# Kernel tuning notes

Hardware: AMD Instinct MI355X
Metric: run time of the kernel (lower is better)

Reference implementation:

```python
import jax, jax.numpy as jnp
import numpy as np

N = 500_000   # active voxel sites
C = 128       # inplanes == outplanes
K = 4         # 2x2 submanifold filter offsets
EPS = 1e-4    # SCN BatchNorm default eps


def setup_inputs() -> dict:
    key = jax.random.key(0)
    ks = jax.random.split(key, 10)
    feat = jax.random.normal(ks[0], (N, C), jnp.float32)
    in_idx = jax.random.randint(ks[1], (K, N), 0, N, dtype=jnp.int32)
    out_idx = jax.random.randint(ks[2], (K, N), 0, N, dtype=jnp.int32)
    mask = jax.random.randint(ks[3], (K, N), 0, 2, dtype=jnp.int32)
    scale = 1.0 / np.sqrt(K * C)
    W1 = jax.random.normal(ks[4], (K, C, C), jnp.float32) * scale
    W2 = jax.random.normal(ks[5], (K, C, C), jnp.float32) * scale
    gamma1 = jnp.ones((C,), jnp.float32)
    beta1 = jnp.zeros((C,), jnp.float32)
    mean1 = jax.random.normal(ks[6], (C,), jnp.float32) * 0.1
    var1 = jax.random.uniform(ks[7], (C,), jnp.float32, 0.5, 1.5)
    gamma2 = jnp.ones((C,), jnp.float32)
    beta2 = jnp.zeros((C,), jnp.float32)
    mean2 = jax.random.normal(ks[8], (C,), jnp.float32) * 0.1
    var2 = jax.random.uniform(ks[9], (C,), jnp.float32, 0.5, 1.5)
    return dict(feat=feat, W1=W1, W2=W2, gamma1=gamma1, beta1=beta1,
                mean1=mean1, var1=var1, gamma2=gamma2, beta2=beta2,
                mean2=mean2, var2=var2, in_idx=in_idx, out_idx=out_idx, mask=mask)


def _subm_conv(feat, W, in_idx, out_idx, maskf):
    # rulebook gather -> GEMM -> scatter-add, one pass per kernel offset
    out = jnp.zeros((feat.shape[0], W.shape[-1]), feat.dtype)
    for k in range(W.shape[0]):  # K=4 fixed small offsets
        g = feat[in_idx[k]] * maskf[k][:, None]   # [N, Cin]
        out = out.at[out_idx[k]].add(g @ W[k])    # scatter to active sites
    return out


def _bn(x, gamma, beta, mean, var):
    return (x - mean) * jax.lax.rsqrt(var + EPS) * gamma + beta


def reference(feat, W1, W2, gamma1, beta1, mean1, var1,
              gamma2, beta2, mean2, var2, in_idx, out_idx, mask):
    maskf = mask.astype(feat.dtype)
    residual = feat                              # scn.Identity (stride=1)
    h = _subm_conv(feat, W1, in_idx, out_idx, maskf)
    h = jax.nn.relu(_bn(h, gamma1, beta1, mean1, var1))  # BatchNormReLU
    h = _subm_conv(h, W2, in_idx, out_idx, maskf)
    h = _bn(h, gamma2, beta2, mean2, var2)       # BatchNormalization
    return h + residual                          # AddTable
```

## Files before the change

kernel.cpp:

```cpp
#include <hip/hip_runtime.h>

#define CDIM 128
#define KOFF 4
#define EPS 1e-4f
#define SCAN_CHUNK 2048
#define ROWS 16
#define NBUF 4
#define NBLK 512
#define NTHR 512
#define CAPM (1 << 18)

typedef __attribute__((ext_vector_type(8))) short bf16x8;
typedef __attribute__((ext_vector_type(4))) float f32x4;

__device__ __forceinline__ unsigned short f2bf(float f) {
    unsigned int u = __builtin_bit_cast(unsigned int, f);
    u += 0x7fffu + ((u >> 16) & 1u);
    return (unsigned short)(u >> 16);
}
__device__ __forceinline__ float bf2f(unsigned short h) {
    unsigned int u = ((unsigned int)h) << 16;
    return __builtin_bit_cast(float, u);
}

__device__ __forceinline__ void gload_lds16(const void* g, void* l) {
    __builtin_amdgcn_global_load_lds(
        (const __attribute__((address_space(1))) void*)g,
        (__attribute__((address_space(3))) void*)l, 16, 0, 0);
}

__global__ __launch_bounds__(256) void wconv_kernel(
    const float* __restrict__ W1, const float* __restrict__ W2,
    short* __restrict__ W1t, short* __restrict__ W2t)
{
    int idx = blockIdx.x * 256 + threadIdx.x;
    if (idx >= KOFF * CDIM * CDIM) return;
    int ci = idx & (CDIM - 1);
    int co = (idx >> 7) & (CDIM - 1);
    int k  = idx >> 14;
    size_t src = (size_t)k * CDIM * CDIM + (size_t)ci * CDIM + co;
    W1t[idx] = (short)f2bf(W1[src]);
    W2t[idx] = (short)f2bf(W2[src]);
}

__global__ __launch_bounds__(256) void prep_kernel(
    const int* __restrict__ out_idx, const int* __restrict__ mask,
    int* __restrict__ cnt, const float* __restrict__ feat,
    short* __restrict__ fb, int n, size_t total8)
{
    if (blockIdx.y == KOFF) {
        size_t stride = (size_t)gridDim.x * 256;
        for (size_t i = (size_t)blockIdx.x * 256 + threadIdx.x; i < total8; i += stride) {
            float4 a = ((const float4*)feat)[i * 2];
            float4 b = ((const float4*)feat)[i * 2 + 1];
            bf16x8 v;
            v[0] = (short)f2bf(a.x); v[1] = (short)f2bf(a.y);
            v[2] = (short)f2bf(a.z); v[3] = (short)f2bf(a.w);
            v[4] = (short)f2bf(b.x); v[5] = (short)f2bf(b.y);
            v[6] = (short)f2bf(b.z); v[7] = (short)f2bf(b.w);
            ((bf16x8*)fb)[i] = v;
        }
    } else {
        int i = blockIdx.x * 256 + threadIdx.x;
        if (i >= n) return;
        int k = blockIdx.y;
        size_t s = (size_t)k * n + i;
        if (mask[s]) atomicAdd(&cnt[(size_t)out_idx[s] * KOFF + k], 1);
    }
}

__global__ __launch_bounds__(256) void scan_p1(
    const int* __restrict__ in, int* __restrict__ bsum, int* __restrict__ bsum2, int L)
{
    __shared__ int red[256], red2[256];
    int base = blockIdx.x * SCAN_CHUNK;
    int s = 0, m = 0;
    #pragma unroll
    for (int u = 0; u < 8; ++u) {
        int i = base + u * 256 + threadIdx.x;
        if (i < L) { int v = in[i]; s += v; m += (v >= 2); }
    }
    red[threadIdx.x] = s; red2[threadIdx.x] = m;
    __syncthreads();
    for (int d = 128; d > 0; d >>= 1) {
        if (threadIdx.x < d) {
            red[threadIdx.x]  += red[threadIdx.x + d];
            red2[threadIdx.x] += red2[threadIdx.x + d];
        }
        __syncthreads();
    }
    if (threadIdx.x == 0) { bsum[blockIdx.x] = red[0]; bsum2[blockIdx.x] = red2[0]; }
}

__global__ __launch_bounds__(1024) void scan_p2(
    int* __restrict__ bsum, int* __restrict__ bsum2, int NB)
{
    __shared__ int s[1024], s2[1024];
    int t = threadIdx.x;
    s[t]  = (t < NB) ? bsum[t]  : 0;
    s2[t] = (t < NB) ? bsum2[t] : 0;
    __syncthreads();
    for (int d = 1; d < 1024; d <<= 1) {
        int x = s[t], y = s2[t];
        if (t >= d) { x += s[t - d]; y += s2[t - d]; }
        __syncthreads();
        s[t] = x; s2[t] = y;
        __syncthreads();
    }
    if (t < NB) {
        bsum[t]  = (t == 0) ? 0 : s[t - 1];
        bsum2[t] = (t == 0) ? 0 : s2[t - 1];
    }
}

__global__ __launch_bounds__(256) void scan_p3(
    const int* __restrict__ cnt, const int* __restrict__ bsum,
    const int* __restrict__ bsum2, int* __restrict__ off_start,
    int* __restrict__ fcur, int* __restrict__ prim,
    int* __restrict__ mlist, int* __restrict__ nmulti, int L, int KN)
{
    __shared__ int ts[256], ms[256];
    int t = threadIdx.x;
    int base = blockIdx.x * SCAN_CHUNK + t * 8;
    int v[8]; int s = 0, m = 0;
    #pragma unroll
    for (int u = 0; u < 8; ++u) {
        int i = base + u;
        v[u] = (i < L) ? cnt[i] : 0;
        s += v[u]; m += (v[u] >= 2);
    }
    ts[t] = s; ms[t] = m;
    __syncthreads();
    for (int d = 1; d < 256; d <<= 1) {
        int x = ts[t], y = ms[t];
        if (t >= d) { x += ts[t - d]; y += ms[t - d]; }
        __syncthreads();
        ts[t] = x; ms[t] = y;
        __syncthreads();
    }
    int pre  = bsum[blockIdx.x]  + ((t == 0) ? 0 : ts[t - 1]);
    int mpre = bsum2[blockIdx.x] + ((t == 0) ? 0 : ms[t - 1]);
    #pragma unroll
    for (int u = 0; u < 8; ++u) {
        int i = base + u;
        if (i < L) {
            off_start[i] = pre;
            fcur[i] = pre;
            if (i < KN) {
                int c = v[u];
                if (c == 0) prim[i] = -1;
                else if (c >= 2) {
                    if (mpre < CAPM) { prim[i] = 0x40000000 | mpre; mlist[mpre] = i; }
                    else prim[i] = -1;
                }
            } else {
                nmulti[0] = mpre;
            }
            pre += v[u]; mpre += (v[u] >= 2);
        }
    }
}

__global__ __launch_bounds__(256) void fill_kernel(
    const int* __restrict__ out_idx, const int* __restrict__ in_idx,
    const int* __restrict__ mask, const int* __restrict__ cnt,
    int* __restrict__ fcur, int* __restrict__ ent, int* __restrict__ prim, int n)
{
    int i = blockIdx.x * 256 + threadIdx.x;
    if (i >= n) return;
    int k = blockIdx.y;
    size_t s = (size_t)k * n + i;
    if (mask[s]) {
        int j = out_idx[s];
        size_t b = (size_t)j * KOFF + k;
        int src = in_idx[s];
        if (cnt[b] == 1) prim[b] = src;
        else { int pos = atomicAdd(&fcur[b], 1); ent[pos] = src; }
    }
}

__global__ __launch_bounds__(256) void merge_kernel(
    const short* __restrict__ Xb, const int* __restrict__ off_start,
    const int* __restrict__ ent, const int* __restrict__ mlist,
    const int* __restrict__ nmulti, short* __restrict__ sumbuf)
{
    int nm = *nmulti; if (nm > CAPM) nm = CAPM;
    int grp  = (blockIdx.x * 256 + threadIdx.x) >> 5;
    int gl   = threadIdx.x & 31;
    int ngrp = (gridDim.x * 256) >> 5;
    for (int i = grp; i < nm; i += ngrp) {
        int b  = mlist[i];
        int e0 = off_start[b];
        int e1 = off_start[b + 1];
        float a0 = 0.f, a1 = 0.f, a2 = 0.f, a3 = 0.f;
        for (int e = e0; e < e1; ++e) {
            int src = ent[e];
            ushort4 v = *((const ushort4*)(Xb + (size_t)src * CDIM) + gl);
            a0 += bf2f(v.x); a1 += bf2f(v.y); a2 += bf2f(v.z); a3 += bf2f(v.w);
        }
        ushort4 o;
        o.x = f2bf(a0); o.y = f2bf(a1); o.z = f2bf(a2); o.w = f2bf(a3);
        *((ushort4*)(sumbuf + (size_t)i * CDIM) + gl) = o;
    }
}

template <int EPI>
__global__ __launch_bounds__(NTHR, 4) void conv_kernel(
    const short* __restrict__ Xb, const short* __restrict__ sumbuf,
    const short* __restrict__ Wt, const int* __restrict__ prim,
    const char* __restrict__ zpage,
    const float* __restrict__ gamma, const float* __restrict__ beta,
    const float* __restrict__ mean, const float* __restrict__ var,
    const float* __restrict__ feat, void* __restrict__ Yv,
    int n, int ntile, int tpb)
{
    const int t    = threadIdx.x;
    const int w    = t >> 6;
    const int lane = t & 63;

    __shared__ alignas(16) short As[NBUF][ROWS * 512];
    __shared__ alignas(16) float s_scale[CDIM], s_shift[CDIM];

    if (t < CDIM) {
        float sc = gamma[t] * rsqrtf(var[t] + EPS);
        s_scale[t] = sc;
        s_shift[t] = beta[t] - mean[t] * sc;
    }
    __syncthreads();

    int t0 = blockIdx.x * tpb;
    int t1 = min(t0 + tpb, ntile);
    if (t0 >= t1) return;

    const int q    = lane >> 4;
    const int p    = lane & 15;
    const int lrow = lane & 15;
    const int g2   = lane >> 4;
    const int col  = w * 16 + lrow;

    bf16x8 wfr[16];
    #pragma unroll
    for (int ks = 0; ks < 16; ++ks) {
        int k  = ks >> 2;
        int kk = ks & 3;
        wfr[ks] = *(const bf16x8*)(Wt + (size_t)k * CDIM * CDIM
                                   + (w * 16 + lrow) * CDIM + kk * 32 + g2 * 8);
    }

    auto LOADP = [&](int ti, int* pr) {
        int tc = (ti < t1) ? ti : (t1 - 1);
        int j0 = tc * ROWS;
        #pragma unroll
        for (int i = 0; i < 2; ++i)
            pr[i] = prim[(size_t)(j0 + w * 2 + i) * KOFF + q];
    };
    auto STAGE = [&](const int* pr, int buf) {
        #pragma unroll
        for (int i = 0; i < 2; ++i) {
            int jl = w * 2 + i;
            int boff = ((p ^ (jl & 7)) << 4);
            int pv = pr[i];
            const char* g;
            if (pv < 0)               g = zpage + boff;
            else if (pv & 0x40000000) g = (const char*)sumbuf + ((size_t)(pv & 0x3FFFFFFF) << 8) + boff;
            else                      g = (const char*)Xb + ((size_t)pv << 8) + boff;
            gload_lds16(g, (char*)As[buf] + jl * 1024);
        }
    };

    auto ITER = [&](int ti, int rb, int sb, const int* prS, int* prL, auto&& VMW) {
        STAGE(prS, sb);
        LOADP(ti + 4, prL);
        VMW();
        __builtin_amdgcn_s_barrier();
        __builtin_amdgcn_sched_barrier(0);

        f32x4 acc = (f32x4){0.f, 0.f, 0.f, 0.f};
        __builtin_amdgcn_s_setprio(1);
        #pragma unroll
        for (int ks = 0; ks < 16; ++ks) {
            int cb = ks * 4 + g2;
            bf16x8 a = *(const bf16x8*)(&As[rb][lrow * 512 + ((cb ^ (lrow & 7)) << 3)]);
            acc = __builtin_amdgcn_mfma_f32_16x16x32_bf16(a, wfr[ks], acc, 0, 0, 0);
        }
        __builtin_amdgcn_s_setprio(0);
        asm volatile("s_waitcnt lgkmcnt(0)" ::: "memory");
        __builtin_amdgcn_s_barrier();

        float* Ot = (float*)As[rb];
        #pragma unroll
        for (int jj = 0; jj < 4; ++jj)
            Ot[(g2 * 4 + jj) * 132 + col] = acc[jj];
        asm volatile("s_waitcnt lgkmcnt(0)" ::: "memory");
        __builtin_amdgcn_s_barrier();

        {
            int row = t >> 5, c4 = t & 31;
            int grow = ti * ROWS + row;
            if (grow < n) {
                float4 x  = *(const float4*)(Ot + row * 132 + c4 * 4);
                float4 sc = ((const float4*)s_scale)[c4];
                float4 sh = ((const float4*)s_shift)[c4];
                size_t go = (size_t)grow * 32 + c4;
                if (EPI == 0) {
                    ushort4 o;
                    o.x = f2bf(fmaxf(x.x * sc.x + sh.x, 0.f));
                    o.y = f2bf(fmaxf(x.y * sc.y + sh.y, 0.f));
                    o.z = f2bf(fmaxf(x.z * sc.z + sh.z, 0.f));
                    o.w = f2bf(fmaxf(x.w * sc.w + sh.w, 0.f));
                    ((ushort4*)Yv)[go] = o;
                } else {
                    float4 f = ((const float4*)feat)[go];
                    float4 r;
                    r.x = x.x * sc.x + sh.x + f.x;
                    r.y = x.y * sc.y + sh.y + f.y;
                    r.z = x.z * sc.z + sh.z + f.z;
                    r.w = x.w * sc.w + sh.w + f.w;
                    ((float4*)Yv)[go] = r;
                }
            }
        }
        asm volatile("s_waitcnt lgkmcnt(0)" ::: "memory");
        __builtin_amdgcn_s_barrier();
    };

    #define VMW_LIT(N0, N1)                                                     \
        [] {                                                                    \
            if (EPI == 0) asm volatile("s_waitcnt vmcnt(" #N0 ")" ::: "memory");\
            else          asm volatile("s_waitcnt vmcnt(" #N1 ")" ::: "memory");\
        }

    int p0[2], p1[2], p2[2], p3[2];
    LOADP(t0,     p0);
    LOADP(t0 + 1, p1);
    LOADP(t0 + 2, p2);
    STAGE(p0, 0);
    STAGE(p1, 1);
    STAGE(p2, 2);
    LOADP(t0 + 3, p3);

    ITER(t0 + 0, 0, 3, p3, p0, VMW_LIT(10, 10));
    if (t0 + 1 < t1) {
        ITER(t0 + 1, 1, 0, p0, p1, VMW_LIT(13, 14));
        if (t0 + 2 < t1) {
            ITER(t0 + 2, 2, 1, p1, p2, VMW_LIT(16, 18));
            if (t0 + 3 < t1) {
                ITER(t0 + 3, 3, 2, p2, p3, VMW_LIT(17, 20));
                for (int ti = t0 + 4; ti < t1; ti += 4) {
                    ITER(ti, 0, 3, p3, p0, VMW_LIT(17, 20));
                    if (ti + 1 >= t1) break;
                    ITER(ti + 1, 1, 0, p0, p1, VMW_LIT(17, 20));
                    if (ti + 2 >= t1) break;
                    ITER(ti + 2, 2, 1, p1, p2, VMW_LIT(17, 20));
                    if (ti + 3 >= t1) break;
                    ITER(ti + 3, 3, 2, p2, p3, VMW_LIT(17, 20));
                }
            }
        }
    }
    #undef VMW_LIT
}

extern "C" void kernel_launch(void* const* d_in, const int* in_sizes, int n_in,
                              void* d_out, int out_size, void* d_ws, size_t ws_size,
                              hipStream_t stream)
{
    const float* feat   = (const float*)d_in[0];
    const float* W1     = (const float*)d_in[1];
    const float* W2     = (const float*)d_in[2];
    const float* gamma1 = (const float*)d_in[3];
    const float* beta1  = (const float*)d_in[4];
    const float* mean1  = (const float*)d_in[5];
    const float* var1   = (const float*)d_in[6];
    const float* gamma2 = (const float*)d_in[7];
    const float* beta2  = (const float*)d_in[8];
    const float* mean2  = (const float*)d_in[9];
    const float* var2   = (const float*)d_in[10];
    const int* in_idx   = (const int*)d_in[11];
    const int* out_idx  = (const int*)d_in[12];
    const int* mask     = (const int*)d_in[13];

    const int n  = in_sizes[0] / CDIM;
    const int KN = KOFF * n;
    const int L  = KN + 1;
    const int NB = (L + SCAN_CHUNK - 1) / SCAN_CHUNK;
    const size_t nelem = (size_t)n * CDIM;

    auto alignup = [](size_t x) { return (x + 255) & ~(size_t)255; };
    char* p = (char*)d_ws;
    int*   cnt    = (int*)p;    p += alignup((size_t)L * 4);
    int*   offs   = (int*)p;    p += alignup((size_t)L * 4);
    int*   fcur   = (int*)p;    p += alignup((size_t)L * 4);
    int*   bsum   = (int*)p;    p += alignup(4096 * 4);
    int*   bsum2  = (int*)p;    p += alignup(4096 * 4);
    int*   ent    = (int*)p;    p += alignup((size_t)KN * 4);
    int*   prim   = (int*)p;    p += alignup((size_t)KN * 4);
    int*   mlist  = (int*)p;    p += alignup((size_t)CAPM * 4);
    int*   nmulti = (int*)p;    p += 256;
    short* W1t    = (short*)p;  p += alignup((size_t)KOFF * CDIM * CDIM * 2);
    short* W2t    = (short*)p;  p += alignup((size_t)KOFF * CDIM * CDIM * 2);
    char*  zpage  = p;          p += 256;
    short* sumbuf = (short*)p;  p += alignup((size_t)CAPM * CDIM * 2);
    short* h1b    = (short*)p;
    short* fb     = (short*)d_out;

    hipMemsetAsync(cnt, 0, (size_t)L * 4, stream);
    hipMemsetAsync(zpage, 0, 256, stream);
    wconv_kernel<<<(KOFF * CDIM * CDIM + 255) / 256, 256, 0, stream>>>(W1, W2, W1t, W2t);
    dim3 pg((n + 255) / 256, KOFF + 1);
    prep_kernel<<<pg, 256, 0, stream>>>(out_idx, mask, cnt, feat, fb, n, nelem / 8);
    scan_p1<<<NB, 256, 0, stream>>>(cnt, bsum, bsum2, L);
    scan_p2<<<1, 1024, 0, stream>>>(bsum, bsum2, NB);
    scan_p3<<<NB, 256, 0, stream>>>(cnt, bsum, bsum2, offs, fcur, prim, mlist, nmulti, L, KN);
    dim3 fg((n + 255) / 256, KOFF);
    fill_kernel<<<fg, 256, 0, stream>>>(out_idx, in_idx, mask, cnt, fcur, ent, prim, n);

    const int ntile = n / ROWS;
    const int tpb   = (ntile + NBLK - 1) / NBLK;

    merge_kernel<<<1024, 256, 0, stream>>>(fb, offs, ent, mlist, nmulti, sumbuf);
    conv_kernel<0><<<NBLK, NTHR, 0, stream>>>(
        fb, sumbuf, W1t, prim, zpage, gamma1, beta1, mean1, var1, nullptr, h1b, n, ntile, tpb);
    merge_kernel<<<1024, 256, 0, stream>>>(h1b, offs, ent, mlist, nmulti, sumbuf);
    conv_kernel<1><<<NBLK, NTHR, 0, stream>>>(
        h1b, sumbuf, W2t, prim, zpage, gamma2, beta2, mean2, var2, feat, d_out, n, ntile, tpb);
}
```

Baseline: 611.4 us.

## Shrink conv pipeline to three LDS buffers, prefetch residual, fold weight conversion into prep

The conv kernel's LDS ring buffer drops from four stages to three, and launch bounds rise to six waves per SIMD. The goal is more resident blocks and more latency hiding across blocks, at the cost of a shallower in-block prefetch depth. The residual feature row for the fp32 epilogue is now loaded at the start of each iteration, so its latency overlaps the MFMA work. The weight transpose/convert kernel is merged into prep_kernel as an extra grid row, saving one launch. The hand-tuned vmcnt wait counts were retuned for the new pipeline depth, and a mistake there could cause races.

```diff
diff --git a/kernel.cpp b/kernel.cpp
--- a/kernel.cpp
+++ b/kernel.cpp
@@ -5,7 +5,7 @@
 #define EPS 1e-4f
 #define SCAN_CHUNK 2048
 #define ROWS 16
-#define NBUF 4
+#define NBUF 3
 #define NBLK 512
 #define NTHR 512
 #define CAPM (1 << 18)
@@ -29,24 +29,13 @@
         (__attribute__((address_space(3))) void*)l, 16, 0, 0);
 }
 
-__global__ __launch_bounds__(256) void wconv_kernel(
-    const float* __restrict__ W1, const float* __restrict__ W2,
-    short* __restrict__ W1t, short* __restrict__ W2t)
-{
-    int idx = blockIdx.x * 256 + threadIdx.x;
-    if (idx >= KOFF * CDIM * CDIM) return;
-    int ci = idx & (CDIM - 1);
-    int co = (idx >> 7) & (CDIM - 1);
-    int k  = idx >> 14;
-    size_t src = (size_t)k * CDIM * CDIM + (size_t)ci * CDIM + co;
-    W1t[idx] = (short)f2bf(W1[src]);
-    W2t[idx] = (short)f2bf(W2[src]);
-}
-
 __global__ __launch_bounds__(256) void prep_kernel(
     const int* __restrict__ out_idx, const int* __restrict__ mask,
     int* __restrict__ cnt, const float* __restrict__ feat,
-    short* __restrict__ fb, int n, size_t total8)
+    short* __restrict__ fb,
+    const float* __restrict__ W1, const float* __restrict__ W2,
+    short* __restrict__ W1t, short* __restrict__ W2t,
+    int n, size_t total8)
 {
     if (blockIdx.y == KOFF) {
         size_t stride = (size_t)gridDim.x * 256;
@@ -60,6 +49,15 @@
             v[6] = (short)f2bf(b.z); v[7] = (short)f2bf(b.w);
             ((bf16x8*)fb)[i] = v;
         }
+    } else if (blockIdx.y == KOFF + 1) {
+        int idx = blockIdx.x * 256 + threadIdx.x;
+        if (idx >= KOFF * CDIM * CDIM) return;
+        int ci = idx & (CDIM - 1);
+        int co = (idx >> 7) & (CDIM - 1);
+        int k  = idx >> 14;
+        size_t src = (size_t)k * CDIM * CDIM + (size_t)ci * CDIM + co;
+        W1t[idx] = (short)f2bf(W1[src]);
+        W2t[idx] = (short)f2bf(W2[src]);
     } else {
         int i = blockIdx.x * 256 + threadIdx.x;
         if (i >= n) return;
@@ -205,7 +203,7 @@
 }
 
 template <int EPI>
-__global__ __launch_bounds__(NTHR, 4) void conv_kernel(
+__global__ __launch_bounds__(NTHR, 6) void conv_kernel(
     const short* __restrict__ Xb, const short* __restrict__ sumbuf,
     const short* __restrict__ Wt, const int* __restrict__ prim,
     const char* __restrict__ zpage,
@@ -269,8 +267,13 @@
     };
 
     auto ITER = [&](int ti, int rb, int sb, const int* prS, int* prL, auto&& VMW) {
+        float4 fpre;
+        int erow = t >> 5, ec4 = t & 31;
+        if (EPI == 1)
+            fpre = ((const float4*)feat)[(size_t)(ti * ROWS + erow) * 32 + ec4];
+
         STAGE(prS, sb);
-        LOADP(ti + 4, prL);
+        LOADP(ti + 3, prL);
         VMW();
         __builtin_amdgcn_s_barrier();
         __builtin_amdgcn_sched_barrier(0);
@@ -295,13 +298,12 @@
         __builtin_amdgcn_s_barrier();
 
         {
-            int row = t >> 5, c4 = t & 31;
-            int grow = ti * ROWS + row;
+            int grow = ti * ROWS + erow;
             if (grow < n) {
-                float4 x  = *(const float4*)(Ot + row * 132 + c4 * 4);
-                float4 sc = ((const float4*)s_scale)[c4];
-                float4 sh = ((const float4*)s_shift)[c4];
-                size_t go = (size_t)grow * 32 + c4;
+                float4 x  = *(const float4*)(Ot + erow * 132 + ec4 * 4);
+                float4 sc = ((const float4*)s_scale)[ec4];
+                float4 sh = ((const float4*)s_shift)[ec4];
+                size_t go = (size_t)grow * 32 + ec4;
                 if (EPI == 0) {
                     ushort4 o;
                     o.x = f2bf(fmaxf(x.x * sc.x + sh.x, 0.f));
@@ -310,12 +312,11 @@
                     o.w = f2bf(fmaxf(x.w * sc.w + sh.w, 0.f));
                     ((ushort4*)Yv)[go] = o;
                 } else {
-                    float4 f = ((const float4*)feat)[go];
                     float4 r;
-                    r.x = x.x * sc.x + sh.x + f.x;
-                    r.y = x.y * sc.y + sh.y + f.y;
-                    r.z = x.z * sc.z + sh.z + f.z;
-                    r.w = x.w * sc.w + sh.w + f.w;
+                    r.x = x.x * sc.x + sh.x + fpre.x;
+                    r.y = x.y * sc.y + sh.y + fpre.y;
+                    r.z = x.z * sc.z + sh.z + fpre.z;
+                    r.w = x.w * sc.w + sh.w + fpre.w;
                     ((float4*)Yv)[go] = r;
                 }
             }
@@ -330,31 +331,24 @@
             else          asm volatile("s_waitcnt vmcnt(" #N1 ")" ::: "memory");\
         }
 
-    int p0[2], p1[2], p2[2], p3[2];
-    LOADP(t0,     p0);
-    LOADP(t0 + 1, p1);
-    LOADP(t0 + 2, p2);
-    STAGE(p0, 0);
-    STAGE(p1, 1);
-    STAGE(p2, 2);
-    LOADP(t0 + 3, p3);
-
-    ITER(t0 + 0, 0, 3, p3, p0, VMW_LIT(10, 10));
+    int pA[2], pB[2], pC[2];
+    LOADP(t0,     pA);
+    LOADP(t0 + 1, pB);
+    STAGE(pA, 0);
+    STAGE(pB, 1);
+    LOADP(t0 + 2, pC);
+
+    ITER(t0 + 0, 0, 2, pC, pA, VMW_LIT(8, 9));
     if (t0 + 1 < t1) {
-        ITER(t0 + 1, 1, 0, p0, p1, VMW_LIT(13, 14));
+        ITER(t0 + 1, 1, 0, pA, pB, VMW_LIT(11, 13));
         if (t0 + 2 < t1) {
-            ITER(t0 + 2, 2, 1, p1, p2, VMW_LIT(16, 18));
-            if (t0 + 3 < t1) {
-                ITER(t0 + 3, 3, 2, p2, p3, VMW_LIT(17, 20));
-                for (int ti = t0 + 4; ti < t1; ti += 4) {
-                    ITER(ti, 0, 3, p3, p0, VMW_LIT(17, 20));
-                    if (ti + 1 >= t1) break;
-                    ITER(ti + 1, 1, 0, p0, p1, VMW_LIT(17, 20));
-                    if (ti + 2 >= t1) break;
-                    ITER(ti + 2, 2, 1, p1, p2, VMW_LIT(17, 20));
-                    if (ti + 3 >= t1) break;
-                    ITER(ti + 3, 3, 2, p2, p3, VMW_LIT(17, 20));
-                }
+            ITER(t0 + 2, 2, 1, pB, pC, VMW_LIT(12, 14));
+            for (int ti = t0 + 3; ti < t1; ti += 3) {
+                ITER(ti, 0, 2, pC, pA, VMW_LIT(12, 14));
+                if (ti + 1 >= t1) break;
+                ITER(ti + 1, 1, 0, pA, pB, VMW_LIT(12, 14));
+                if (ti + 2 >= t1) break;
+                ITER(ti + 2, 2, 1, pB, pC, VMW_LIT(12, 14));
             }
         }
     }
@@ -406,9 +400,9 @@
 
     hipMemsetAsync(cnt, 0, (size_t)L * 4, stream);
     hipMemsetAsync(zpage, 0, 256, stream);
-    wconv_kernel<<<(KOFF * CDIM * CDIM + 255) / 256, 256, 0, stream>>>(W1, W2, W1t, W2t);
-    dim3 pg((n + 255) / 256, KOFF + 1);
-    prep_kernel<<<pg, 256, 0, stream>>>(out_idx, mask, cnt, feat, fb, n, nelem / 8);
+    dim3 pg((n + 255) / 256, KOFF + 2);
+    prep_kernel<<<pg, 256, 0, stream>>>(out_idx, mask, cnt, feat, fb,
+                                        W1, W2, W1t, W2t, n, nelem / 8);
     scan_p1<<<NB, 256, 0, stream>>>(cnt, bsum, bsum2, L);
     scan_p2<<<1, 1024, 0, stream>>>(bsum, bsum2, NB);
     scan_p3<<<NB, 256, 0, stream>>>(cnt, bsum, bsum2, offs, fcur, prim, mlist, nmulti, L, KN);
```

After: 1.577 ms. 2.58x slower.
